# Kernel optimization log

Hardware: AMD Instinct MI355X
Metric: run time of the kernel (lower is better)

## Reference

```python
import jax, jax.numpy as jnp
import numpy as np

B, NA, LAT, HID, AF, L = 512, 58, 64, 128, 10, 2
N = B * NA
E = N * 16


def silu(x):
    return x * jax.nn.sigmoid(x)


def setup_inputs() -> dict:
    key = jax.random.key(0)
    ks = list(jax.random.split(key, 32))

    def p(k, shape, fan_in):
        return jax.random.normal(k, shape, jnp.float32) / np.sqrt(fan_in)

    inp = {
        "z": jax.random.normal(ks[0], (B, LAT), jnp.float32),
        "atom_types": jax.random.uniform(ks[1], (N, AF), jnp.float32),
        "edge_index": jax.random.randint(ks[2], (2, E), 0, N, jnp.int64),
        "init_coords": jax.random.normal(ks[3], (NA, 3), jnp.float32) * 0.1,
        "latent_w": p(ks[4], (LAT, HID), LAT), "latent_b": jnp.zeros((HID,), jnp.float32),
        "atom_w": p(ks[5], (AF, HID), AF), "atom_b": jnp.zeros((HID,), jnp.float32),
        # per-layer stacked params (leading dim = num_layers)
        "edge_w1": p(ks[6], (L, 2 * HID + 1, HID), 2 * HID + 1), "edge_b1": jnp.zeros((L, HID), jnp.float32),
        "edge_w2": p(ks[7], (L, HID, HID), HID), "edge_b2": jnp.zeros((L, HID), jnp.float32),
        "node_w1": p(ks[8], (L, 2 * HID, HID), 2 * HID), "node_b1": jnp.zeros((L, HID), jnp.float32),
        "node_w2": p(ks[9], (L, HID, HID), HID), "node_b2": jnp.zeros((L, HID), jnp.float32),
        "coord_w1": p(ks[10], (L, HID, HID), HID), "coord_b1": jnp.zeros((L, HID), jnp.float32),
        "coord_w2": p(ks[11], (L, HID, 1), HID),  # no bias
        "ln_g": jnp.ones((L, HID), jnp.float32), "ln_b": jnp.zeros((L, HID), jnp.float32),
        "head_w1": p(ks[12], (HID, HID // 2), HID), "head_b1": jnp.zeros((HID // 2,), jnp.float32),
        "head_w2": p(ks[13], (HID // 2, 3), HID // 2), "head_b2": jnp.zeros((3,), jnp.float32),
    }
    return inp


def _layer(h, pos, row, col, ew1, eb1, ew2, eb2, nw1, nb1, nw2, nb2, cw1, cb1, cw2, lg, lb):
    n = h.shape[0]
    xi, xj = h[row], h[col]                      # [E,HID] gathers
    rel = pos[row] - pos[col]                    # [E,3]
    d2 = jnp.clip(jnp.sum(rel * rel, axis=-1, keepdims=True), 1e-6, 1e6)
    ef = jnp.concatenate([xi, xj, d2], axis=-1)  # [E,2H+1]
    m = silu(silu(ef @ ew1 + eb1) @ ew2 + eb2)   # edge MLP messages [E,HID]
    agg = jax.ops.segment_sum(m, row, num_segments=n)
    hn = silu(jnp.concatenate([h, agg], axis=-1) @ nw1 + nb1) @ nw2 + nb2
    mu = jnp.mean(hn, axis=-1, keepdims=True)
    var = jnp.mean((hn - mu) ** 2, axis=-1, keepdims=True)
    hn = (hn - mu) * jax.lax.rsqrt(var + 1e-5) * lg + lb
    cw = jnp.clip(silu(m @ cw1 + cb1) @ cw2, -1.0, 1.0)  # [E,1]
    upd = jax.ops.segment_sum(cw * rel, row, num_segments=n)  # [N,3]
    deg = jax.ops.segment_sum(jnp.ones((row.shape[0],), pos.dtype), row, num_segments=n)[:, None]
    pos_new = pos + upd / (deg + 1e-6)
    return hn, pos_new


def reference(z, atom_types, edge_index, init_coords, latent_w, latent_b, atom_w, atom_b,
              edge_w1, edge_b1, edge_w2, edge_b2, node_w1, node_b1, node_w2, node_b2,
              coord_w1, coord_b1, coord_w2, ln_g, ln_b, head_w1, head_b1, head_w2, head_b2):
    b = z.shape[0]
    na = init_coords.shape[0]
    n = b * na
    h = z @ latent_w + latent_b                              # [B,HID]
    h = jnp.broadcast_to(h[:, None, :], (b, na, h.shape[-1])).reshape(n, -1)
    h = h + (atom_types @ atom_w + atom_b)
    pos = jnp.broadcast_to(init_coords[None], (b, na, 3)).reshape(n, 3)
    row, col = edge_index[0], edge_index[1]
    for l in range(edge_w1.shape[0]):
        h, pos = _layer(h, pos, row, col,
                        edge_w1[l], edge_b1[l], edge_w2[l], edge_b2[l],
                        node_w1[l], node_b1[l], node_w2[l], node_b2[l],
                        coord_w1[l], coord_b1[l], coord_w2[l], ln_g[l], ln_b[l])
    delta = silu(h @ head_w1 + head_b1) @ head_w2 + head_b2
    return pos + delta
```

## Files before the change

### kernel.cpp

```cpp
#include <hip/hip_runtime.h>
#include <hip/hip_bf16.h>

#define BB 512
#define NA 58
#define LAT 64
#define HID 128
#define AF 10
#define NL 2
#define NN (BB*NA)
#define NE (NN*16)
#define ET 64
#define NTILE (NE/ET)

typedef __attribute__((ext_vector_type(8))) short s8;
typedef __attribute__((ext_vector_type(4))) float f4;

struct CvtDesc {
    const void* src[24];
    float*      dst[24];
    int         len[24];
};

struct PackJobs {
    const float* src[11];
    short*       dst[11];
    int          K[11];
    int          mode[11];
};

__device__ __forceinline__ float siluf(float x) {
    return x * __builtin_amdgcn_rcpf(1.0f + __expf(-x));
}

__device__ __forceinline__ short f2b(float x) {
    __hip_bfloat16 b = __float2bfloat16(x);
    return *(short*)&b;
}

__device__ __forceinline__ float b2f(short s) {
    return __uint_as_float(((unsigned int)(unsigned short)s) << 16);
}

__global__ void k_detect(const unsigned short* __restrict__ z16,
                         const unsigned int* __restrict__ e32,
                         int* __restrict__ flags) {
    __shared__ int sbf, si64;
    if (threadIdx.x == 0) { sbf = 0; si64 = 0; }
    __syncthreads();
    int c1 = 0, c2 = 0;
    for (int i = threadIdx.x; i < 1024; i += 256) {
        unsigned short v = z16[2*i];
        int e = (v >> 7) & 0xFF;
        if (e >= 100 && e <= 140) c1++;
        if (e32[2*i + 1] == 0u) c2++;
    }
    atomicAdd(&sbf, c1);
    atomicAdd(&si64, c2);
    __syncthreads();
    if (threadIdx.x == 0) {
        flags[0] = (sbf  > 600) ? 1 : 0;
        flags[1] = (si64 > 600) ? 1 : 0;
    }
}

__global__ void k_convert(CvtDesc d, const int* __restrict__ flags) {
    int a = blockIdx.y;
    int i = blockIdx.x * blockDim.x + threadIdx.x;
    int n = d.len[a];
    if (i >= n) return;
    if (flags[0]) {
        d.dst[a][i] = __bfloat162float(((const __hip_bfloat16*)d.src[a])[i]);
    } else {
        d.dst[a][i] = ((const float*)d.src[a])[i];
    }
}

__global__ void k_packall(PackJobs pj) {
    int j = blockIdx.y;
    int idx = blockIdx.x * 256 + threadIdx.x;
    const float* w = pj.src[j];
    short* o = pj.dst[j];
    int mode = pj.mode[j];
    if (mode == 0) {
        int K = pj.K[j];
        if (idx >= 128*K) return;
        int jj = idx & 7;
        int l  = (idx >> 3) & 63;
        int rest = idx >> 9;
        int KC = K >> 5;
        int kc = rest % KC;
        int nt = rest / KC;
        int n = nt*16 + (l & 15);
        int k = kc*32 + (l >> 4)*8 + jj;
        o[idx] = f2b(w[k*128 + n]);
    } else if (mode == 1) {
        if (idx >= 32768) return;
        int jj = idx & 7;
        int l  = (idx >> 3) & 63;
        int rest = idx >> 9;
        int kc = rest & 3;
        int nt = rest >> 2;
        int n = nt*16 + (l & 15);
        int k = kc*32 + (l >> 4)*8 + jj;
        float v = (n < 128) ? w[k*128 + n] : w[(128 + k)*128 + (n - 128)];
        o[idx] = f2b(v);
    } else {
        if (idx >= 8192) return;
        int jj = idx & 7;
        int l  = (idx >> 3) & 63;
        int rest = idx >> 9;
        int kc = rest & 3;
        int nt = rest >> 2;
        int n = nt*16 + (l & 15);
        int k = kc*32 + (l >> 4)*8 + jj;
        o[idx] = f2b(w[k*64 + n]);
    }
}

__global__ void k_hist(const int* __restrict__ eidx, const int* __restrict__ flags,
                       int* __restrict__ cnt) {
    int e = blockIdx.x * 256 + threadIdx.x;
    if (e >= NE) return;
    int is64 = flags[1];
    int r = eidx[is64 ? 2*(long)e : (long)e];
    atomicAdd(&cnt[r], 1);
}

__global__ __launch_bounds__(1024) void k_scan(const int* __restrict__ cnt,
                                               int* __restrict__ rowStart,
                                               int* __restrict__ cursor) {
    __shared__ int part[1024];
    int t = threadIdx.x;
    int base = t * 29;
    int loc[29];
    int s = 0;
    #pragma unroll
    for (int i = 0; i < 29; ++i) { loc[i] = s; s += cnt[base + i]; }
    part[t] = s;
    __syncthreads();
    for (int d = 1; d < 1024; d <<= 1) {
        int v = (t >= d) ? part[t - d] : 0;
        __syncthreads();
        part[t] += v;
        __syncthreads();
    }
    int pre = (t == 0) ? 0 : part[t - 1];
    #pragma unroll
    for (int i = 0; i < 29; ++i) {
        int v = pre + loc[i];
        rowStart[base + i] = v;
        cursor[base + i] = v;
    }
    if (t == 1023) rowStart[NN] = pre + s;
}

__global__ void k_scatter(const int* __restrict__ eidx, const int* __restrict__ flags,
                          int* __restrict__ cursor,
                          int* __restrict__ rS, int* __restrict__ cS) {
    int e = blockIdx.x * 256 + threadIdx.x;
    if (e >= NE) return;
    int is64 = flags[1];
    long ge = e, gc = (long)e + NE;
    int r = eidx[is64 ? 2*ge : ge];
    int c = eidx[is64 ? 2*gc : gc];
    int p = atomicAdd(&cursor[r], 1);
    rS[p] = r; cS[p] = c;
}

__global__ __launch_bounds__(256) void k_init3(
    const float* __restrict__ z, const float* __restrict__ lw,
    const float* __restrict__ lbz,
    const float* __restrict__ at,
    const float* __restrict__ aw, const float* __restrict__ ab,
    const float* __restrict__ ic,
    float* __restrict__ pos, short* __restrict__ hb,
    const short* __restrict__ wcat0, const float* __restrict__ b10,
    short* __restrict__ H1, float* __restrict__ agg, float* __restrict__ upd)
{
    __shared__ short x[64][136];
    __shared__ float awS[AF][HID];
    __shared__ float atS[64][AF+2];
    __shared__ float zbS[3][LAT];
    __shared__ float hzS[3][HID];
    const int tid = threadIdx.x;
    const int n0 = blockIdx.x * 64;
    const int b0 = n0 / NA;
    const int nb = (n0 + 63) / NA - b0 + 1;

    for (int i = tid; i < AF*HID; i += 256) awS[i/HID][i%HID] = aw[i];
    for (int i = tid; i < 64*AF; i += 256)
        atS[i/AF][i%AF] = at[(long)(n0 + i/AF)*AF + i%AF];
    for (int i = tid; i < nb*LAT; i += 256) {
        int bi = i / LAT, k = i - bi*LAT;
        int bidx = b0 + bi;
        zbS[bi][k] = (bidx < BB) ? z[bidx*LAT + k] : 0.f;
    }
    __syncthreads();

    for (int i = tid; i < nb*HID; i += 256) {
        int bi = i / HID, c = i - bi*HID;
        float acc = lbz[c];
        #pragma unroll
        for (int k = 0; k < LAT; ++k) acc += zbS[bi][k] * lw[k*HID + c];
        hzS[bi][c] = acc;
    }
    __syncthreads();

    #pragma unroll
    for (int it = 0; it < 32; ++it) {
        int idx = it*256 + tid;
        int r = idx >> 7, c = idx & 127;
        int n = n0 + r;
        float v = hzS[n/NA - b0][c] + ab[c];
        #pragma unroll
        for (int f = 0; f < AF; ++f) v += atS[r][f]*awS[f][c];
        short s = f2b(v);
        x[r][c] = s;
        hb[(long)n*HID + c] = s;
    }
    if (tid < 192) {
        int i = tid/3, d = tid - i*3;
        int n = n0 + i;
        pos[n*3 + d] = ic[(n % NA)*3 + d];
        upd[n*3 + d] = 0.f;
    }
    {
        f4* a4 = (f4*)(agg + (long)n0*HID);
        for (int j = tid; j < 64*HID/4; j += 256) a4[j] = (f4)0.f;
    }
    __syncthreads();

    const int l = tid & 63, w = tid >> 6;
    const int l16 = l & 15, quad = l >> 4;
    f4 acc[4][4];
    #pragma unroll
    for (int mt = 0; mt < 4; ++mt)
        #pragma unroll
        for (int nt4 = 0; nt4 < 4; ++nt4) acc[mt][nt4] = (f4)0.f;
    #pragma unroll
    for (int kc = 0; kc < 4; ++kc) {
        s8 a[4];
        #pragma unroll
        for (int mt = 0; mt < 4; ++mt)
            a[mt] = *(const s8*)&x[mt*16 + l16][kc*32 + quad*8];
        #pragma unroll
        for (int nt4 = 0; nt4 < 4; ++nt4) {
            int nt = w*4 + nt4;
            s8 b = *(const s8*)(wcat0 + (((size_t)nt*4 + kc)*64 + l)*8);
            #pragma unroll
            for (int mt = 0; mt < 4; ++mt)
                acc[mt][nt4] = __builtin_amdgcn_mfma_f32_16x16x32_bf16(a[mt], b, acc[mt][nt4], 0, 0, 0);
        }
    }
    #pragma unroll
    for (int nt4 = 0; nt4 < 4; ++nt4) {
        int col = (w*4 + nt4)*16 + l16;
        float bias = (col < 128) ? b10[col] : 0.f;
        #pragma unroll
        for (int mt = 0; mt < 4; ++mt)
            #pragma unroll
            for (int i = 0; i < 4; ++i) {
                int row = mt*16 + quad*4 + i;
                H1[(long)(n0 + row)*256 + col] = f2b(acc[mt][nt4][i] + bias);
            }
    }
}

__global__ __launch_bounds__(256, 3) void k_edge_os(
    const short* __restrict__ H1,
    const int* __restrict__ rS, const int* __restrict__ cS,
    const float* __restrict__ pos,
    const float* __restrict__ w1c,
    const short* __restrict__ w2p, const float* __restrict__ b2,
    const short* __restrict__ c1p, const float* __restrict__ cb1,
    const float* __restrict__ cw2,
    float* __restrict__ agg, float* __restrict__ upd)
{
    __shared__ short t1[ET][136];
    __shared__ int   rIs[ET], cIs[ET];
    __shared__ float sred[ET];

    const int tid = threadIdx.x;
    const int l = tid & 63, w = tid >> 6;
    const int l16 = l & 15, quad = l >> 4;
    const int c0 = (2*w)*16 + l16, c1c = (2*w+1)*16 + l16;
    const int half = tid >> 7, ch = tid & 127;
    const int q = tid & 15;
    const int esub = tid >> 4;
    const int T = blockIdx.x;

    f4 acc[4][2];

    float wv[8];
    #pragma unroll
    for (int j = 0; j < 8; ++j) wv[j] = w1c[q*8 + j];

    const long eb = (long)T * ET;
    if (tid < ET) sred[tid] = 0.f;
    #pragma unroll
    for (int it = 0; it < 4; ++it) {
        int e = esub + 16*it;
        int r = rS[eb + e], c = cS[eb + e];
        float rx = pos[r*3+0] - pos[c*3+0];
        float ry = pos[r*3+1] - pos[c*3+1];
        float rz = pos[r*3+2] - pos[c*3+2];
        float d2 = fminf(fmaxf(rx*rx + ry*ry + rz*rz, 1e-6f), 1e6f);
        s8 va = *(const s8*)(H1 + (long)r*256 + q*8);
        s8 vb = *(const s8*)(H1 + (long)c*256 + 128 + q*8);
        s8 o;
        #pragma unroll
        for (int j = 0; j < 8; ++j)
            o[j] = f2b(siluf(b2f(va[j]) + b2f(vb[j]) + d2*wv[j]));
        *(s8*)&t1[e][q*8] = o;
        if (q == 0) { rIs[e] = r; cIs[e] = c; }
    }
    __syncthreads();

    #pragma unroll
    for (int mt = 0; mt < 4; ++mt) { acc[mt][0] = (f4)0.f; acc[mt][1] = (f4)0.f; }
    {
        const short* wb0 = w2p + ((size_t)(2*w)*4*64 + l)*8;
        const short* wb1 = w2p + ((size_t)(2*w+1)*4*64 + l)*8;
        s8 b0 = *(const s8*)wb0;
        s8 b1 = *(const s8*)wb1;
        #pragma unroll
        for (int it = 0; it < 4; ++it) {
            s8 nb0 = b0, nb1 = b1;
            if (it < 3) {
                nb0 = *(const s8*)(wb0 + (size_t)(it+1)*512);
                nb1 = *(const s8*)(wb1 + (size_t)(it+1)*512);
            }
            #pragma unroll
            for (int mt = 0; mt < 4; ++mt) {
                s8 a = *(const s8*)&t1[mt*16 + l16][it*32 + quad*8];
                acc[mt][0] = __builtin_amdgcn_mfma_f32_16x16x32_bf16(a, b0, acc[mt][0], 0, 0, 0);
                acc[mt][1] = __builtin_amdgcn_mfma_f32_16x16x32_bf16(a, b1, acc[mt][1], 0, 0, 0);
            }
            b0 = nb0; b1 = nb1;
        }
    }
    __syncthreads();

    short (*mm)[136] = t1;
    {
        const float bia2_0 = b2[c0], bia2_1 = b2[c1c];
        #pragma unroll
        for (int mt = 0; mt < 4; ++mt) {
            #pragma unroll
            for (int i = 0; i < 4; ++i) {
                int row = mt*16 + quad*4 + i;
                mm[row][c0]  = f2b(siluf(acc[mt][0][i] + bia2_0));
                mm[row][c1c] = f2b(siluf(acc[mt][1][i] + bia2_1));
            }
        }
    }
    __syncthreads();

    {
        int e0 = half * 32;
        int cur = rIs[e0];
        float a = 0.f;
        #pragma unroll
        for (int e = e0; e < e0 + 32; ++e) {
            int r = rIs[e];
            if (r != cur) {
                atomicAdd(&agg[(long)cur*HID + ch], a);
                a = 0.f; cur = r;
            }
            a += b2f(mm[e][ch]);
        }
        atomicAdd(&agg[(long)cur*HID + ch], a);
    }
    {
        #pragma unroll
        for (int mt = 0; mt < 4; ++mt) { acc[mt][0] = (f4)0.f; acc[mt][1] = (f4)0.f; }
        const short* cb0 = c1p + ((size_t)(2*w)*4*64 + l)*8;
        const short* cb1p_ = c1p + ((size_t)(2*w+1)*4*64 + l)*8;
        s8 b0 = *(const s8*)cb0;
        s8 b1 = *(const s8*)cb1p_;
        #pragma unroll
        for (int kc = 0; kc < 4; ++kc) {
            s8 nb0 = b0, nb1 = b1;
            if (kc < 3) {
                nb0 = *(const s8*)(cb0 + (size_t)(kc+1)*512);
                nb1 = *(const s8*)(cb1p_ + (size_t)(kc+1)*512);
            }
            #pragma unroll
            for (int mt = 0; mt < 4; ++mt) {
                s8 a = *(const s8*)&mm[mt*16 + l16][kc*32 + quad*8];
                acc[mt][0] = __builtin_amdgcn_mfma_f32_16x16x32_bf16(a, b0, acc[mt][0], 0, 0, 0);
                acc[mt][1] = __builtin_amdgcn_mfma_f32_16x16x32_bf16(a, b1, acc[mt][1], 0, 0, 0);
            }
            b0 = nb0; b1 = nb1;
        }
        const float biac_0 = cb1[c0], biac_1 = cb1[c1c];
        const float cw0    = cw2[c0], cw1v   = cw2[c1c];
        #pragma unroll
        for (int mt = 0; mt < 4; ++mt) {
            #pragma unroll
            for (int i = 0; i < 4; ++i) {
                float p = siluf(acc[mt][0][i] + biac_0) * cw0
                        + siluf(acc[mt][1][i] + biac_1) * cw1v;
                p += __shfl_xor(p, 1);
                p += __shfl_xor(p, 2);
                p += __shfl_xor(p, 4);
                p += __shfl_xor(p, 8);
                if (l16 == 0) {
                    int row = mt*16 + quad*4 + i;
                    atomicAdd(&sred[row], p);
                }
            }
        }
    }
    int   ur = 0;
    float urx = 0.f, ury = 0.f, urz = 0.f;
    if (tid < ET) {
        ur = rIs[tid];
        int uc = cIs[tid];
        urx = pos[ur*3+0] - pos[uc*3+0];
        ury = pos[ur*3+1] - pos[uc*3+1];
        urz = pos[ur*3+2] - pos[uc*3+2];
    }
    __syncthreads();

    if (tid < ET) {
        float cwv = fminf(fmaxf(sred[tid], -1.f), 1.f);
        atomicAdd(&upd[ur*3+0], cwv*urx);
        atomicAdd(&upd[ur*3+1], cwv*ury);
        atomicAdd(&upd[ur*3+2], cwv*urz);
    }
}

__global__ __launch_bounds__(256) void k_node_mfma(
    short* __restrict__ hb, float* __restrict__ agg,
    const short* __restrict__ w1p, const float* __restrict__ b1n,
    const short* __restrict__ w2p, const float* __restrict__ b2n,
    const float* __restrict__ lg, const float* __restrict__ lb,
    float* __restrict__ pos, float* __restrict__ upd,
    const int* __restrict__ rowStart,
    const short* __restrict__ wcatn, const float* __restrict__ b1next,
    short* __restrict__ H1,
    const short* __restrict__ hw1p, const float* __restrict__ hb1,
    const float* __restrict__ hw2, const float* __restrict__ hb2,
    void* __restrict__ out, const int* __restrict__ flags)
{
    __shared__ short x[64][264];
    __shared__ short t1[64][144];
    __shared__ float mus[64], rstds[64];
    __shared__ float posS[64][3];
    float (*hn)[132] = (float (*)[132])&x[0][0];
    float (*hid)[68] = (float (*)[68])&x[0][0];

    const int tid = threadIdx.x;
    const int n0 = blockIdx.x * 64;

    #pragma unroll
    for (int it = 0; it < 4; ++it) {
        int idx = it*256 + tid;
        int e = idx >> 4, qq = idx & 15;
        *(int4*)&x[e][qq*8] = *(const int4*)(hb + (long)(n0+e)*HID + qq*8);
    }
    #pragma unroll
    for (int it = 0; it < 8; ++it) {
        int idx = it*256 + tid;
        int e = idx >> 5, qq = idx & 31;
        float4 v = *(const float4*)(agg + (long)(n0+e)*HID + qq*4);
        short4 sv;
        sv.x = f2b(v.x); sv.y = f2b(v.y); sv.z = f2b(v.z); sv.w = f2b(v.w);
        *(short4*)&x[e][128 + qq*4] = sv;
    }
    __syncthreads();

    {
        f4* a4 = (f4*)(agg + (long)n0*HID);
        for (int j = tid; j < 64*HID/4; j += 256) a4[j] = (f4)0.f;
    }

    const int l = tid & 63, w = tid >> 6;
    const int l16 = l & 15, quad = l >> 4;
    const int nt0 = 2*w, nt1 = 2*w + 1;
    const int c0 = nt0*16 + l16, c1c = nt1*16 + l16;

    {
        f4 acc[4][2];
        #pragma unroll
        for (int mt = 0; mt < 4; ++mt) { acc[mt][0] = (f4)0.f; acc[mt][1] = (f4)0.f; }
        #pragma unroll
        for (int kc = 0; kc < 8; ++kc) {
            s8 b0  = *(const s8*)(w1p + (((size_t)nt0*8 + kc)*64 + l)*8);
            s8 b1f = *(const s8*)(w1p + (((size_t)nt1*8 + kc)*64 + l)*8);
            #pragma unroll
            for (int mt = 0; mt < 4; ++mt) {
                s8 a = *(const s8*)&x[mt*16 + l16][kc*32 + quad*8];
                acc[mt][0] = __builtin_amdgcn_mfma_f32_16x16x32_bf16(a, b0,  acc[mt][0], 0, 0, 0);
                acc[mt][1] = __builtin_amdgcn_mfma_f32_16x16x32_bf16(a, b1f, acc[mt][1], 0, 0, 0);
            }
        }
        float bia0 = b1n[c0], bia1 = b1n[c1c];
        #pragma unroll
        for (int mt = 0; mt < 4; ++mt) {
            #pragma unroll
            for (int i = 0; i < 4; ++i) {
                int row = mt*16 + quad*4 + i;
                t1[row][c0]  = f2b(siluf(acc[mt][0][i] + bia0));
                t1[row][c1c] = f2b(siluf(acc[mt][1][i] + bia1));
            }
        }
    }
    __syncthreads();

    {
        f4 acc[4][2];
        #pragma unroll
        for (int mt = 0; mt < 4; ++mt) { acc[mt][0] = (f4)0.f; acc[mt][1] = (f4)0.f; }
        #pragma unroll
        for (int kc = 0; kc < 4; ++kc) {
            s8 b0  = *(const s8*)(w2p + (((size_t)nt0*4 + kc)*64 + l)*8);
            s8 b1f = *(const s8*)(w2p + (((size_t)nt1*4 + kc)*64 + l)*8);
            #pragma unroll
            for (int mt = 0; mt < 4; ++mt) {
                s8 a = *(const s8*)&t1[mt*16 + l16][kc*32 + quad*8];
                acc[mt][0] = __builtin_amdgcn_mfma_f32_16x16x32_bf16(a, b0,  acc[mt][0], 0, 0, 0);
                acc[mt][1] = __builtin_amdgcn_mfma_f32_16x16x32_bf16(a, b1f, acc[mt][1], 0, 0, 0);
            }
        }
        float bia0 = b2n[c0], bia1 = b2n[c1c];
        __syncthreads();
        #pragma unroll
        for (int mt = 0; mt < 4; ++mt) {
            #pragma unroll
            for (int i = 0; i < 4; ++i) {
                int row = mt*16 + quad*4 + i;
                hn[row][c0]  = acc[mt][0][i] + bia0;
                hn[row][c1c] = acc[mt][1][i] + bia1;
            }
        }
    }
    __syncthreads();

    {
        int r = tid >> 2, part = tid & 3;
        float s = 0.f, qv = 0.f;
        #pragma unroll
        for (int j = 0; j < 32; ++j) {
            float v = hn[r][part + 4*j];
            s += v; qv += v*v;
        }
        s += __shfl_xor(s, 1); qv += __shfl_xor(qv, 1);
        s += __shfl_xor(s, 2); qv += __shfl_xor(qv, 2);
        if (part == 0) {
            float mu = s * (1.0f/HID);
            float var = qv * (1.0f/HID) - mu*mu;
            mus[r] = mu;
            rstds[r] = rsqrtf(var + 1e-5f);
        }
    }
    __syncthreads();

    #pragma unroll
    for (int it = 0; it < 32; ++it) {
        int idx = it*256 + tid;
        int r = idx >> 7, c = idx & 127;
        float v = (hn[r][c] - mus[r]) * rstds[r] * lg[c] + lb[c];
        short s = f2b(v);
        hb[(long)(n0 + r)*HID + c] = s;
        t1[r][c] = s;
    }
    if (tid < 192) {
        int i = tid / 3, d = tid - i*3;
        int n = n0 + i;
        float dg = (float)(rowStart[n+1] - rowStart[n]);
        float np = pos[n*3+d] + upd[n*3+d] / (dg + 1e-6f);
        pos[n*3+d] = np;
        posS[i][d] = np;
        upd[n*3+d] = 0.f;
    }
    __syncthreads();

    if (wcatn) {
        f4 acc[4][4];
        #pragma unroll
        for (int mt = 0; mt < 4; ++mt)
            #pragma unroll
            for (int nt4 = 0; nt4 < 4; ++nt4) acc[mt][nt4] = (f4)0.f;
        #pragma unroll
        for (int kc = 0; kc < 4; ++kc) {
            s8 a[4];
            #pragma unroll
            for (int mt = 0; mt < 4; ++mt)
                a[mt] = *(const s8*)&t1[mt*16 + l16][kc*32 + quad*8];
            #pragma unroll
            for (int nt4 = 0; nt4 < 4; ++nt4) {
                int nt = w*4 + nt4;
                s8 b = *(const s8*)(wcatn + (((size_t)nt*4 + kc)*64 + l)*8);
                #pragma unroll
                for (int mt = 0; mt < 4; ++mt)
                    acc[mt][nt4] = __builtin_amdgcn_mfma_f32_16x16x32_bf16(a[mt], b, acc[mt][nt4], 0, 0, 0);
            }
        }
        #pragma unroll
        for (int nt4 = 0; nt4 < 4; ++nt4) {
            int col = (w*4 + nt4)*16 + l16;
            float bias = (col < 128) ? b1next[col] : 0.f;
            #pragma unroll
            for (int mt = 0; mt < 4; ++mt)
                #pragma unroll
                for (int i = 0; i < 4; ++i) {
                    int row = mt*16 + quad*4 + i;
                    H1[(long)(n0 + row)*256 + col] = f2b(acc[mt][nt4][i] + bias);
                }
        }
    } else {
        f4 acc[4];
        #pragma unroll
        for (int mt = 0; mt < 4; ++mt) acc[mt] = (f4)0.f;
        #pragma unroll
        for (int kc = 0; kc < 4; ++kc) {
            s8 b = *(const s8*)(hw1p + (((size_t)w*4 + kc)*64 + l)*8);
            #pragma unroll
            for (int mt = 0; mt < 4; ++mt) {
                s8 a = *(const s8*)&t1[mt*16 + l16][kc*32 + quad*8];
                acc[mt] = __builtin_amdgcn_mfma_f32_16x16x32_bf16(a, b, acc[mt], 0, 0, 0);
            }
        }
        int col = w*16 + l16;
        float bias = hb1[col];
        #pragma unroll
        for (int mt = 0; mt < 4; ++mt)
            #pragma unroll
            for (int i = 0; i < 4; ++i) {
                int row = mt*16 + quad*4 + i;
                hid[row][col] = siluf(acc[mt][i] + bias);
            }
        __syncthreads();
        if (tid < 192) {
            int r = tid / 3, cc = tid - r*3;
            float a2 = hb2[cc];
            #pragma unroll
            for (int k = 0; k < 64; ++k) a2 += hid[r][k] * hw2[k*3 + cc];
            int n = n0 + r;
            float v = posS[r][cc] + a2;
            if (flags[0]) ((__hip_bfloat16*)out)[n*3+cc] = __float2bfloat16(v);
            else          ((float*)out)[n*3+cc] = v;
        }
    }
}

extern "C" void kernel_launch(void* const* d_in, const int* in_sizes, int n_in,
                              void* d_out, int out_size, void* d_ws, size_t ws_size,
                              hipStream_t stream)
{
    (void)in_sizes; (void)n_in; (void)out_size; (void)ws_size;

    int* flags = (int*)d_ws;
    float* base = (float*)d_ws;
    size_t off = 64;
    auto alloc = [&](size_t n) { float* p = base + off; off += (n + 63) & ~63ull; return p; };

    static const int aidx[24] = {0,1,3,4,5,6,7,8,9,10,11,12,13,14,15,16,17,18,19,20,21,22,23,24};
    static const int alen[24] = {
        BB*LAT, NN*AF, NA*3, LAT*HID, HID, AF*HID, HID,
        NL*257*HID, NL*HID, NL*HID*HID, NL*HID,
        NL*256*HID, NL*HID, NL*HID*HID, NL*HID,
        NL*HID*HID, NL*HID, NL*HID, NL*HID, NL*HID,
        HID*64, 64, 64*3, 3
    };
    CvtDesc cd;
    float* fp[24];
    for (int a = 0; a < 24; ++a) {
        fp[a] = alloc((size_t)alen[a]);
        cd.src[a] = d_in[aidx[a]];
        cd.dst[a] = fp[a];
        cd.len[a] = alen[a];
    }
    float* agg = alloc((size_t)NN*HID);
    float* pos = alloc((size_t)NN*3);
    float* upd = alloc((size_t)NN*3);
    short* hb  = (short*)alloc((size_t)NN*HID/2);
    short* H1  = (short*)alloc((size_t)NN*256/2);
    short* wcatp = (short*)alloc((size_t)NL*32768/2);
    short* w2p = (short*)alloc((size_t)NL*16384/2);
    short* c1p = (short*)alloc((size_t)NL*16384/2);
    short* nw1p = (short*)alloc((size_t)NL*32768/2);
    short* nw2p = (short*)alloc((size_t)NL*16384/2);
    short* hw1p = (short*)alloc((size_t)8192/2);
    int* cnt      = (int*)alloc((size_t)NN);
    int* rowStart = (int*)alloc((size_t)NN + 1);
    int* cursor   = (int*)alloc((size_t)NN);
    int* rS       = (int*)alloc((size_t)NE);
    int* cS       = (int*)alloc((size_t)NE);
    const int* eidx = (const int*)d_in[2];

    k_detect<<<1, 256, 0, stream>>>((const unsigned short*)d_in[0],
                                    (const unsigned int*)d_in[2], flags);
    k_convert<<<dim3((NN*AF + 255)/256, 24), 256, 0, stream>>>(cd, flags);

    PackJobs pj;
    for (int l = 0; l < NL; ++l) {
        int b5 = l*5;
        pj.src[b5+0] = fp[7]  + (size_t)l*257*HID; pj.dst[b5+0] = wcatp + (size_t)l*32768; pj.K[b5+0] = 256; pj.mode[b5+0] = 1;
        pj.src[b5+1] = fp[9]  + (size_t)l*HID*HID; pj.dst[b5+1] = w2p   + (size_t)l*16384; pj.K[b5+1] = 128; pj.mode[b5+1] = 0;
        pj.src[b5+2] = fp[15] + (size_t)l*HID*HID; pj.dst[b5+2] = c1p   + (size_t)l*16384; pj.K[b5+2] = 128; pj.mode[b5+2] = 0;
        pj.src[b5+3] = fp[11] + (size_t)l*256*HID; pj.dst[b5+3] = nw1p  + (size_t)l*32768; pj.K[b5+3] = 256; pj.mode[b5+3] = 0;
        pj.src[b5+4] = fp[13] + (size_t)l*HID*HID; pj.dst[b5+4] = nw2p  + (size_t)l*16384; pj.K[b5+4] = 128; pj.mode[b5+4] = 0;
    }
    pj.src[10] = fp[20]; pj.dst[10] = hw1p; pj.K[10] = 128; pj.mode[10] = 2;
    k_packall<<<dim3(128, 11), 256, 0, stream>>>(pj);

    hipMemsetAsync(cnt, 0, (size_t)NN*sizeof(int), stream);
    k_hist<<<(NE + 255)/256, 256, 0, stream>>>(eidx, flags, cnt);
    k_scan<<<1, 1024, 0, stream>>>(cnt, rowStart, cursor);
    k_scatter<<<(NE + 255)/256, 256, 0, stream>>>(eidx, flags, cursor, rS, cS);

    k_init3<<<NN/64, 256, 0, stream>>>(fp[0], fp[3], fp[4],
                                       fp[1], fp[5], fp[6], fp[2], pos, hb,
                                       wcatp, fp[8], H1, agg, upd);

    for (int l = 0; l < NL; ++l) {
        k_edge_os<<<NTILE, 256, 0, stream>>>(H1, rS, cS, pos,
            fp[7] + (size_t)l*257*HID + 256*HID,
            w2p + (size_t)l*16384, fp[10] + (size_t)l*HID,
            c1p + (size_t)l*16384, fp[16] + (size_t)l*HID,
            fp[17] + (size_t)l*HID,
            agg, upd);
        const short* wcatn = (l+1 < NL) ? (wcatp + (size_t)(l+1)*32768) : nullptr;
        const float* b1nx  = (l+1 < NL) ? (fp[8] + (size_t)(l+1)*HID) : fp[8];
        k_node_mfma<<<NN/64, 256, 0, stream>>>(hb, agg,
            nw1p + (size_t)l*32768, fp[12] + (size_t)l*HID,
            nw2p + (size_t)l*16384, fp[14] + (size_t)l*HID,
            fp[18] + (size_t)l*HID, fp[19] + (size_t)l*HID,
            pos, upd, rowStart, wcatn, b1nx, H1,
            hw1p, fp[21], fp[22], fp[23], d_out, flags);
    }
}
```

Baseline: 571.4 us.

## Process two edge tiles per block, prefetching second tile's gathers

```diff
diff --git a/kernel.cpp b/kernel.cpp
--- a/kernel.cpp
+++ b/kernel.cpp
@@ -276,8 +276,8 @@
     const float* __restrict__ cw2,
     float* __restrict__ agg, float* __restrict__ upd)
 {
-    __shared__ short t1[ET][136];
-    __shared__ int   rIs[ET], cIs[ET];
+    __shared__ short t1[2][ET][136];
+    __shared__ int   rIs[2][ET], cIs[2][ET];
     __shared__ float sred[ET];
 
     const int tid = threadIdx.x;
@@ -287,7 +287,6 @@
     const int half = tid >> 7, ch = tid & 127;
     const int q = tid & 15;
     const int esub = tid >> 4;
-    const int T = blockIdx.x;
 
     f4 acc[4][2];
 
@@ -295,12 +294,15 @@
     #pragma unroll
     for (int j = 0; j < 8; ++j) wv[j] = w1c[q*8 + j];
 
-    const long eb = (long)T * ET;
+    const long eb0 = (long)blockIdx.x * (2*ET);
+    const long eb1 = eb0 + ET;
+
     if (tid < ET) sred[tid] = 0.f;
+
     #pragma unroll
     for (int it = 0; it < 4; ++it) {
         int e = esub + 16*it;
-        int r = rS[eb + e], c = cS[eb + e];
+        int r = rS[eb0 + e], c = cS[eb0 + e];
         float rx = pos[r*3+0] - pos[c*3+0];
         float ry = pos[r*3+1] - pos[c*3+1];
         float rz = pos[r*3+2] - pos[c*3+2];
@@ -311,8 +313,22 @@
         #pragma unroll
         for (int j = 0; j < 8; ++j)
             o[j] = f2b(siluf(b2f(va[j]) + b2f(vb[j]) + d2*wv[j]));
-        *(s8*)&t1[e][q*8] = o;
-        if (q == 0) { rIs[e] = r; cIs[e] = c; }
+        *(s8*)&t1[0][e][q*8] = o;
+        if (q == 0) { rIs[0][e] = r; cIs[0][e] = c; }
+    }
+    float pd2[4];
+    s8 va1[4], vb1[4];
+    #pragma unroll
+    for (int it = 0; it < 4; ++it) {
+        int e = esub + 16*it;
+        int r = rS[eb1 + e], c = cS[eb1 + e];
+        if (q == 0) { rIs[1][e] = r; cIs[1][e] = c; }
+        float rx = pos[r*3+0] - pos[c*3+0];
+        float ry = pos[r*3+1] - pos[c*3+1];
+        float rz = pos[r*3+2] - pos[c*3+2];
+        pd2[it] = fminf(fmaxf(rx*rx + ry*ry + rz*rz, 1e-6f), 1e6f);
+        va1[it] = *(const s8*)(H1 + (long)r*256 + q*8);
+        vb1[it] = *(const s8*)(H1 + (long)c*256 + 128 + q*8);
     }
     __syncthreads();
 
@@ -332,7 +348,7 @@
             }
             #pragma unroll
             for (int mt = 0; mt < 4; ++mt) {
-                s8 a = *(const s8*)&t1[mt*16 + l16][it*32 + quad*8];
+                s8 a = *(const s8*)&t1[0][mt*16 + l16][it*32 + quad*8];
                 acc[mt][0] = __builtin_amdgcn_mfma_f32_16x16x32_bf16(a, b0, acc[mt][0], 0, 0, 0);
                 acc[mt][1] = __builtin_amdgcn_mfma_f32_16x16x32_bf16(a, b1, acc[mt][1], 0, 0, 0);
             }
@@ -341,7 +357,7 @@
     }
     __syncthreads();
 
-    short (*mm)[136] = t1;
+    short (*mm0)[136] = t1[0];
     {
         const float bia2_0 = b2[c0], bia2_1 = b2[c1c];
         #pragma unroll
@@ -349,25 +365,34 @@
             #pragma unroll
             for (int i = 0; i < 4; ++i) {
                 int row = mt*16 + quad*4 + i;
-                mm[row][c0]  = f2b(siluf(acc[mt][0][i] + bia2_0));
-                mm[row][c1c] = f2b(siluf(acc[mt][1][i] + bia2_1));
-            }
-        }
+                mm0[row][c0]  = f2b(siluf(acc[mt][0][i] + bia2_0));
+                mm0[row][c1c] = f2b(siluf(acc[mt][1][i] + bia2_1));
+            }
+        }
+    }
+    #pragma unroll
+    for (int it = 0; it < 4; ++it) {
+        int e = esub + 16*it;
+        s8 o;
+        #pragma unroll
+        for (int j = 0; j < 8; ++j)
+            o[j] = f2b(siluf(b2f(va1[it][j]) + b2f(vb1[it][j]) + pd2[it]*wv[j]));
+        *(s8*)&t1[1][e][q*8] = o;
     }
     __syncthreads();
 
     {
         int e0 = half * 32;
-        int cur = rIs[e0];
+        int cur = rIs[0][e0];
         float a = 0.f;
         #pragma unroll
         for (int e = e0; e < e0 + 32; ++e) {
-            int r = rIs[e];
+            int r = rIs[0][e];
             if (r != cur) {
                 atomicAdd(&agg[(long)cur*HID + ch], a);
                 a = 0.f; cur = r;
             }
-            a += b2f(mm[e][ch]);
+            a += b2f(mm0[e][ch]);
         }
         atomicAdd(&agg[(long)cur*HID + ch], a);
     }
@@ -387,7 +412,7 @@
             }
             #pragma unroll
             for (int mt = 0; mt < 4; ++mt) {
-                s8 a = *(const s8*)&mm[mt*16 + l16][kc*32 + quad*8];
+                s8 a = *(const s8*)&mm0[mt*16 + l16][kc*32 + quad*8];
                 acc[mt][0] = __builtin_amdgcn_mfma_f32_16x16x32_bf16(a, b0, acc[mt][0], 0, 0, 0);
                 acc[mt][1] = __builtin_amdgcn_mfma_f32_16x16x32_bf16(a, b1, acc[mt][1], 0, 0, 0);
             }
@@ -412,22 +437,137 @@
             }
         }
     }
-    int   ur = 0;
-    float urx = 0.f, ury = 0.f, urz = 0.f;
+    int   ur0 = 0;
+    float ux0 = 0.f, uy0 = 0.f, uz0 = 0.f;
     if (tid < ET) {
-        ur = rIs[tid];
-        int uc = cIs[tid];
-        urx = pos[ur*3+0] - pos[uc*3+0];
-        ury = pos[ur*3+1] - pos[uc*3+1];
-        urz = pos[ur*3+2] - pos[uc*3+2];
+        ur0 = rIs[0][tid];
+        int uc = cIs[0][tid];
+        ux0 = pos[ur0*3+0] - pos[uc*3+0];
+        uy0 = pos[ur0*3+1] - pos[uc*3+1];
+        uz0 = pos[ur0*3+2] - pos[uc*3+2];
     }
     __syncthreads();
 
     if (tid < ET) {
         float cwv = fminf(fmaxf(sred[tid], -1.f), 1.f);
-        atomicAdd(&upd[ur*3+0], cwv*urx);
-        atomicAdd(&upd[ur*3+1], cwv*ury);
-        atomicAdd(&upd[ur*3+2], cwv*urz);
+        atomicAdd(&upd[ur0*3+0], cwv*ux0);
+        atomicAdd(&upd[ur0*3+1], cwv*uy0);
+        atomicAdd(&upd[ur0*3+2], cwv*uz0);
+        sred[tid] = 0.f;
+    }
+
+    #pragma unroll
+    for (int mt = 0; mt < 4; ++mt) { acc[mt][0] = (f4)0.f; acc[mt][1] = (f4)0.f; }
+    {
+        const short* wb0 = w2p + ((size_t)(2*w)*4*64 + l)*8;
+        const short* wb1 = w2p + ((size_t)(2*w+1)*4*64 + l)*8;
+        s8 b0 = *(const s8*)wb0;
+        s8 b1 = *(const s8*)wb1;
+        #pragma unroll
+        for (int it = 0; it < 4; ++it) {
+            s8 nb0 = b0, nb1 = b1;
+            if (it < 3) {
+                nb0 = *(const s8*)(wb0 + (size_t)(it+1)*512);
+                nb1 = *(const s8*)(wb1 + (size_t)(it+1)*512);
+            }
+            #pragma unroll
+            for (int mt = 0; mt < 4; ++mt) {
+                s8 a = *(const s8*)&t1[1][mt*16 + l16][it*32 + quad*8];
+                acc[mt][0] = __builtin_amdgcn_mfma_f32_16x16x32_bf16(a, b0, acc[mt][0], 0, 0, 0);
+                acc[mt][1] = __builtin_amdgcn_mfma_f32_16x16x32_bf16(a, b1, acc[mt][1], 0, 0, 0);
+            }
+            b0 = nb0; b1 = nb1;
+        }
+    }
+    __syncthreads();
+
+    short (*mm1)[136] = t1[1];
+    {
+        const float bia2_0 = b2[c0], bia2_1 = b2[c1c];
+        #pragma unroll
+        for (int mt = 0; mt < 4; ++mt) {
+            #pragma unroll
+            for (int i = 0; i < 4; ++i) {
+                int row = mt*16 + quad*4 + i;
+                mm1[row][c0]  = f2b(siluf(acc[mt][0][i] + bia2_0));
+                mm1[row][c1c] = f2b(siluf(acc[mt][1][i] + bia2_1));
+            }
+        }
+    }
+    __syncthreads();
+
+    {
+        int e0 = half * 32;
+        int cur = rIs[1][e0];
+        float a = 0.f;
+        #pragma unroll
+        for (int e = e0; e < e0 + 32; ++e) {
+            int r = rIs[1][e];
+            if (r != cur) {
+                atomicAdd(&agg[(long)cur*HID + ch], a);
+                a = 0.f; cur = r;
+            }
+            a += b2f(mm1[e][ch]);
+        }
+        atomicAdd(&agg[(long)cur*HID + ch], a);
+    }
+    {
+        #pragma unroll
+        for (int mt = 0; mt < 4; ++mt) { acc[mt][0] = (f4)0.f; acc[mt][1] = (f4)0.f; }
+        const short* cb0 = c1p + ((size_t)(2*w)*4*64 + l)*8;
+        const short* cb1p_ = c1p + ((size_t)(2*w+1)*4*64 + l)*8;
+        s8 b0 = *(const s8*)cb0;
+        s8 b1 = *(const s8*)cb1p_;
+        #pragma unroll
+        for (int kc = 0; kc < 4; ++kc) {
+            s8 nb0 = b0, nb1 = b1;
+            if (kc < 3) {
+                nb0 = *(const s8*)(cb0 + (size_t)(kc+1)*512);
+                nb1 = *(const s8*)(cb1p_ + (size_t)(kc+1)*512);
+            }
+            #pragma unroll
+            for (int mt = 0; mt < 4; ++mt) {
+                s8 a = *(const s8*)&mm1[mt*16 + l16][kc*32 + quad*8];
+                acc[mt][0] = __builtin_amdgcn_mfma_f32_16x16x32_bf16(a, b0, acc[mt][0], 0, 0, 0);
+                acc[mt][1] = __builtin_amdgcn_mfma_f32_16x16x32_bf16(a, b1, acc[mt][1], 0, 0, 0);
+            }
+            b0 = nb0; b1 = nb1;
+        }
+        const float biac_0 = cb1[c0], biac_1 = cb1[c1c];
+        const float cw0    = cw2[c0], cw1v   = cw2[c1c];
+        #pragma unroll
+        for (int mt = 0; mt < 4; ++mt) {
+            #pragma unroll
+            for (int i = 0; i < 4; ++i) {
+                float p = siluf(acc[mt][0][i] + biac_0) * cw0
+                        + siluf(acc[mt][1][i] + biac_1) * cw1v;
+                p += __shfl_xor(p, 1);
+                p += __shfl_xor(p, 2);
+                p += __shfl_xor(p, 4);
+                p += __shfl_xor(p, 8);
+                if (l16 == 0) {
+                    int row = mt*16 + quad*4 + i;
+                    atomicAdd(&sred[row], p);
+                }
+            }
+        }
+    }
+    int   ur1 = 0;
+    float ux1 = 0.f, uy1 = 0.f, uz1 = 0.f;
+    if (tid < ET) {
+        ur1 = rIs[1][tid];
+        int uc = cIs[1][tid];
+        ux1 = pos[ur1*3+0] - pos[uc*3+0];
+        uy1 = pos[ur1*3+1] - pos[uc*3+1];
+        uz1 = pos[ur1*3+2] - pos[uc*3+2];
+    }
+    __syncthreads();
+
+    if (tid < ET) {
+        float cwv = fminf(fmaxf(sred[tid], -1.f), 1.f);
+        atomicAdd(&upd[ur1*3+0], cwv*ux1);
+        atomicAdd(&upd[ur1*3+1], cwv*uy1);
+        atomicAdd(&upd[ur1*3+2], cwv*uz1);
     }
 }
 
@@ -717,7 +857,7 @@
                                        wcatp, fp[8], H1, agg, upd);
 
     for (int l = 0; l < NL; ++l) {
-        k_edge_os<<<NTILE, 256, 0, stream>>>(H1, rS, cS, pos,
+        k_edge_os<<<NTILE/2, 256, 0, stream>>>(H1, rS, cS, pos,
             fp[7] + (size_t)l*257*HID + 256*HID,
             w2p + (size_t)l*16384, fp[10] + (size_t)l*HID,
             c1p + (size_t)l*16384, fp[16] + (size_t)l*HID,
```

After: 571.2 us. About the same (-0.0%).
